# Kernel optimization log

Hardware: AMD Instinct MI355X
Metric: run time of the kernel (lower is better)

The kernel has to match this reference:

```python
import jax, jax.numpy as jnp
import numpy as np

H = W = 56
WS = 7          # window size
SHIFT = 3       # shift size
HEADS = 4
DIM = 128
NUM_MLP = 512
EPS = 1e-5


def _build_rel_index():
    ch = np.arange(WS)
    cw = np.arange(WS)
    coords = np.stack(np.meshgrid(ch, cw, indexing='ij')).reshape(2, -1)  # [2,49]
    rel = coords[:, :, None] - coords[:, None, :]                         # [2,49,49]
    rel = rel.transpose(1, 2, 0)
    rel[:, :, 0] += WS - 1
    rel[:, :, 1] += WS - 1
    rel[:, :, 0] *= 2 * WS - 1
    return rel.sum(-1).astype(np.int32)                                   # [49,49]


def _build_attn_mask():
    mask = np.zeros((H, W), dtype=np.float32)
    slices = (slice(0, -WS), slice(-WS, -SHIFT), slice(-SHIFT, None))
    cnt = 0
    for hs in slices:
        for ws_ in slices:
            mask[hs, ws_] = cnt
            cnt += 1
    nH, nW = H // WS, W // WS
    mw = mask.reshape(nH, WS, nW, WS).transpose(0, 2, 1, 3).reshape(nH * nW, WS * WS)
    am = mw[:, None, :] - mw[:, :, None]
    return np.where(am != 0, -100.0, 0.0).astype(np.float32)              # [64,49,49]


def setup_inputs() -> dict:
    key = jax.random.key(0)
    ks = jax.random.split(key, 8)
    B = 64
    s = 0.02
    return {
        'x': jax.random.normal(ks[0], (B, H * W, DIM), jnp.float32),
        'ln1_g': jnp.ones((DIM,), jnp.float32),
        'ln1_b': jnp.zeros((DIM,), jnp.float32),
        'eca_w': jax.random.normal(ks[1], (3, DIM, 1), jnp.float32) * s,
        'qkv_w': jax.random.normal(ks[2], (DIM, 3 * DIM), jnp.float32) * s,
        'qkv_b': jnp.zeros((3 * DIM,), jnp.float32),
        'rel_bias_table': jax.random.normal(ks[3], ((2 * WS - 1) ** 2, HEADS), jnp.float32) * s,
        'proj_w': jax.random.normal(ks[4], (DIM, DIM), jnp.float32) * s,
        'proj_b': jnp.zeros((DIM,), jnp.float32),
        'ln2_g': jnp.ones((DIM,), jnp.float32),
        'ln2_b': jnp.zeros((DIM,), jnp.float32),
        'mlp_w1': jax.random.normal(ks[5], (DIM, NUM_MLP), jnp.float32) * s,
        'mlp_b1': jnp.zeros((NUM_MLP,), jnp.float32),
        'mlp_w2': jax.random.normal(ks[6], (NUM_MLP, DIM), jnp.float32) * s,
        'mlp_b2': jnp.zeros((DIM,), jnp.float32),
        'attn_mask': jnp.asarray(_build_attn_mask()),
        'rel_index': jnp.asarray(_build_rel_index()),
    }


def _layer_norm(x, g, b):
    mu = x.mean(-1, keepdims=True)
    var = jnp.mean((x - mu) ** 2, -1, keepdims=True)
    return (x - mu) * jax.lax.rsqrt(var + EPS) * g + b


def _forward(x, ln1_g, ln1_b, eca_w, qkv_w, qkv_b, rel_bias_table, proj_w, proj_b,
             ln2_g, ln2_b, mlp_w1, mlp_b1, mlp_w2, mlp_b2, attn_mask, rel_index):
    B, L, C = x.shape
    nH, nW = H // WS, W // WS
    nwin = nH * nW
    hd = C // HEADS
    scale = hd ** -0.5

    x_skip = x
    xs = _layer_norm(x, ln1_g, ln1_b)
    x4 = xs.reshape(B, H, W, C)

    # Efficient channel attention (faithful: Conv1D over a length-1 steps axis,
    # 'same' padding -> only the center kernel tap contributes; gate is [B,1,1])
    sq = x4.mean((1, 2))[:, None, :]                                  # [B,1,C]
    gate = jax.lax.conv_general_dilated(
        sq, eca_w, (1,), 'SAME', dimension_numbers=('NWC', 'WIO', 'NWC'))  # [B,1,1]
    gate = jax.nn.sigmoid(gate)
    cattn = (x4 * gate[:, :, :, None]).reshape(B, H * W, C)

    # cyclic shift + window partition (batch-major, standard Swin layout)
    shifted = jnp.roll(x4, (-SHIFT, -SHIFT), (1, 2))
    xw = shifted.reshape(B, nH, WS, nW, WS, C).transpose(0, 1, 3, 2, 4, 5)
    xw = xw.reshape(B * nwin, WS * WS, C)                              # [Bn,49,C]

    # window attention with gathered relative position bias
    qkv = (xw @ qkv_w + qkv_b).reshape(-1, WS * WS, 3, HEADS, hd)
    qkv = qkv.transpose(2, 0, 3, 1, 4)                                 # [3,Bn,h,49,hd]
    q, k, v = qkv[0], qkv[1], qkv[2]
    attn = jnp.einsum('bhqd,bhkd->bhqk', q * scale, k)                 # [Bn,h,49,49]
    bias = rel_bias_table[rel_index.reshape(-1)]                       # [49*49,h]
    bias = bias.reshape(WS * WS, WS * WS, HEADS).transpose(2, 0, 1)    # [h,49,49]
    attn = attn + bias[None]
    attn = attn.reshape(B, nwin, HEADS, WS * WS, WS * WS) + attn_mask[None, :, None]
    attn = jax.nn.softmax(attn.reshape(-1, HEADS, WS * WS, WS * WS), -1)
    out = jnp.einsum('bhqk,bhkd->bqhd', attn, v).reshape(-1, WS * WS, C)
    out = out @ proj_w + proj_b                                        # [Bn,49,C]

    # window reverse + reverse shift
    out = out.reshape(B, nH, nW, WS, WS, C).transpose(0, 1, 3, 2, 4, 5)
    out = out.reshape(B, H, W, C)
    out = jnp.roll(out, (SHIFT, SHIFT), (1, 2)).reshape(B, H * W, C)

    x = x_skip + out + cattn
    x_skip = x
    xn = _layer_norm(x, ln2_g, ln2_b)
    h1 = jax.nn.gelu(xn @ mlp_w1 + mlp_b1, approximate=False)
    return x_skip + (h1 @ mlp_w2 + mlp_b2)


def reference(x, ln1_g, ln1_b, eca_w, qkv_w, qkv_b, rel_bias_table, proj_w, proj_b,
              ln2_g, ln2_b, mlp_w1, mlp_b1, mlp_w2, mlp_b2, attn_mask, rel_index):
    return _forward(x, ln1_g, ln1_b, eca_w, qkv_w, qkv_b, rel_bias_table, proj_w,
                    proj_b, ln2_g, ln2_b, mlp_w1, mlp_b1, mlp_w2, mlp_b2,
                    attn_mask, rel_index)
```

## Files before the change

kernel.cpp:

```cpp
#include <hip/hip_runtime.h>
#include <hip/hip_bf16.h>
#include <math.h>

#define B_    64
#define Himg  56
#define Wimg  56
#define L_    (Himg*Wimg)
#define WS_   7
#define SHIFT 3
#define NWIN  64
#define NTOK  49
#define HEADS 4
#define HD    32
#define DIM   128
#define NMLP  512
#define EPS   1e-5f
#define SCALE 0.17677669529663687f

typedef __hip_bfloat16 bf16;
typedef __attribute__((ext_vector_type(8))) short short8;
typedef __attribute__((ext_vector_type(4))) float floatx4;
typedef __attribute__((ext_vector_type(4))) unsigned short ushort4v;
#define MFMA16(a, b, c) __builtin_amdgcn_mfma_f32_16x16x32_bf16(a, b, c, 0, 0, 0)

__device__ float g_gacc[B_];
__device__ __align__(16) unsigned short g_w1t[NMLP * DIM];
__device__ __align__(16) unsigned short g_w2t[DIM * NMLP];
__device__ __align__(16) unsigned short g_qkvwt[3 * DIM * DIM];
__device__ __align__(16) unsigned short g_pwt[DIM * DIM];
__device__ float g_combo[NWIN * HEADS * NTOK * NTOK];

__device__ __forceinline__ float us2f(unsigned short u) {
  return __uint_as_float(((unsigned int)u) << 16);
}
__device__ __forceinline__ unsigned short f2us(float f) {
  unsigned int x = __float_as_uint(f);
  x += 0x7fffu + ((x >> 16) & 1u);
  return (unsigned short)(x >> 16);
}
__device__ __forceinline__ bool is_bf(const void* ones) {
  return ((const unsigned int*)ones)[0] == 0x3F803F80u;
}
template<bool BF>
__device__ __forceinline__ float ldf(const void* p, size_t i) {
  if (BF) return __bfloat162float(((const bf16*)p)[i]);
  return ((const float*)p)[i];
}
template<bool BF>
__device__ __forceinline__ floatx4 ld4(const void* p, size_t i) {
  if (BF) {
    const ushort4v u = *(const ushort4v*)((const unsigned short*)p + i);
    floatx4 r = {us2f(u.x), us2f(u.y), us2f(u.z), us2f(u.w)};
    return r;
  }
  return *(const floatx4*)((const float*)p + i);
}
template<bool BF>
__device__ __forceinline__ void st4(void* p, size_t i, floatx4 v) {
  if (BF) {
    ushort4v u = {f2us(v.x), f2us(v.y), f2us(v.z), f2us(v.w)};
    *(ushort4v*)((unsigned short*)p + i) = u;
  } else {
    *(floatx4*)((float*)p + i) = v;
  }
}
__device__ __forceinline__ float gelu_t(float x) {
  float y = 0.7978845608028654f * (x + 0.044715f * x * x * x);
  y = fminf(fmaxf(y, -15.f), 15.f);
  const float e = __expf(2.f * y);
  return 0.5f * x * (1.f + (e - 1.f) / (e + 1.f));
}

template<bool BF>
__global__ void k_prep(const void* __restrict__ w1, const void* __restrict__ w2,
                       const void* __restrict__ qkvw, const void* __restrict__ pw,
                       const void* __restrict__ rbt, const void* __restrict__ amask,
                       const int* __restrict__ ridx, const void* __restrict__ ones) {
  if (is_bf(ones) != BF) return;
  const int bid = blockIdx.x, tid = threadIdx.x;
  if (bid == 0 && tid < B_) g_gacc[tid] = 0.f;
  if (bid < 256) {
    const int idx = bid * 256 + tid;
    { const int k = idx >> 9, n = idx & 511; g_w1t[n * DIM + k] = f2us(ldf<BF>(w1, idx)); }
    { const int k = idx >> 7, n = idx & 127; g_w2t[n * NMLP + k] = f2us(ldf<BF>(w2, idx)); }
  } else if (bid < 448) {
    const int idx = (bid - 256) * 256 + tid;
    { const int k = idx / 384, n = idx % 384; g_qkvwt[n * DIM + k] = f2us(ldf<BF>(qkvw, idx)); }
    if (idx < DIM * DIM) {
      const int k = idx >> 7, n = idx & 127;
      g_pwt[n * DIM + k] = f2us(ldf<BF>(pw, idx));
    }
  } else {
    const int wh_ = bid - 448;
    const int widx = wh_ >> 2, h = wh_ & 3;
    for (int idx = tid; idx < NTOK * NTOK; idx += 256) {
      g_combo[(size_t)wh_ * (NTOK * NTOK) + idx] =
          ldf<BF>(rbt, (size_t)ridx[idx] * HEADS + h) +
          ldf<BF>(amask, (size_t)widx * (NTOK * NTOK) + idx);
    }
  }
}

template<bool BF>
__global__ void k_gate_partial(const void* __restrict__ x,
                               const void* __restrict__ ln1_g,
                               const void* __restrict__ ln1_b,
                               const void* __restrict__ eca_w) {
  if (is_bf(ln1_g) != BF) return;
  const int b = blockIdx.x;
  const int lane = threadIdx.x & 63;
  const int wave = threadIdx.x >> 6;
  const int c4 = (lane & 31) * 4;
  const floatx4 g4  = ld4<BF>(ln1_g, c4);
  const floatx4 be4 = ld4<BF>(ln1_b, c4);
  const floatx4 w4  = ld4<BF>(eca_w, DIM + c4);
  float acc = 0.f;
  const int t0 = blockIdx.y * 8 + wave * 2 + (lane >> 5);
  for (int t = t0; t < L_; t += 64) {
    const floatx4 v = ld4<BF>(x, ((size_t)b * L_ + t) * DIM + c4);
    float s = v.x + v.y + v.z + v.w;
    float s2 = v.x * v.x + v.y * v.y + v.z * v.z + v.w * v.w;
    #pragma unroll
    for (int m = 1; m <= 16; m <<= 1) {
      s  += __shfl_xor(s,  m, 64);
      s2 += __shfl_xor(s2, m, 64);
    }
    const float mu = s * (1.f / DIM);
    const float rs = rsqrtf(s2 * (1.f / DIM) - mu * mu + EPS);
    acc += ((v.x - mu) * rs * g4.x + be4.x) * w4.x
         + ((v.y - mu) * rs * g4.y + be4.y) * w4.y
         + ((v.z - mu) * rs * g4.z + be4.z) * w4.z
         + ((v.w - mu) * rs * g4.w + be4.w) * w4.w;
  }
  #pragma unroll
  for (int m = 1; m <= 32; m <<= 1) acc += __shfl_xor(acc, m, 64);
  if (lane == 0) atomicAdd(&g_gacc[b], acc);
}

template<bool BF>
__global__ __launch_bounds__(512, 4) void k_attn_mfma(
    const void* __restrict__ x,
    const void* __restrict__ ln1_g, const void* __restrict__ ln1_b,
    const void* __restrict__ qkv_b, const void* __restrict__ proj_b,
    void* __restrict__ x2) {
  if (is_bf(ln1_g) != BF) return;
  __shared__ __align__(16) unsigned short q_s[NTOK * 136];
  __shared__ __align__(16) unsigned short k_s[NTOK * 136];
  __shared__ __align__(16) unsigned short xno[NTOK * 136];
  __shared__ __align__(16) unsigned short vt[128 * 72];
  __shared__ __align__(16) unsigned short Pb[8 * 16 * 40];
  __shared__ float mu[NTOK], rs[NTOK];
  unsigned short* o_s = q_s;

  const int tid = threadIdx.x;
  const int bw = blockIdx.x;
  const int b = bw >> 6, widx = bw & 63;
  const int wh = widx >> 3, wc = widx & 7;
  const int w = tid >> 6, l = tid & 63;
  const int pair = w >> 1, p = w & 1;
  const int lr = l & 15, lq = l >> 4;

  for (int idx = tid; idx < 128 * 16; idx += 512)
    vt[(idx >> 4) * 72 + 48 + (idx & 15)] = 0;
  for (int idx = tid; idx < NTOK * 32; idx += 512) {
    const int i = idx >> 5, c4 = (idx & 31) * 4;
    const int r = i / 7, qq = i % 7;
    const int oh = (wh * 7 + r + SHIFT) % Himg;
    const int ow = (wc * 7 + qq + SHIFT) % Wimg;
    const floatx4 v = ld4<BF>(x, ((size_t)b * L_ + oh * Wimg + ow) * DIM + c4);
    ushort4v u = {f2us(v.x), f2us(v.y), f2us(v.z), f2us(v.w)};
    *(ushort4v*)&xno[i * 136 + c4] = u;
  }
  __syncthreads();
  {
    const int i = tid >> 3, c0 = (tid & 7) * 16;
    if (i < NTOK) {
      const short8 r0 = *(const short8*)&xno[i * 136 + c0];
      const short8 r1 = *(const short8*)&xno[i * 136 + c0 + 8];
      float s = 0.f, s2 = 0.f;
      #pragma unroll
      for (int j = 0; j < 8; j++) {
        const float a = us2f((unsigned short)r0[j]);
        const float c = us2f((unsigned short)r1[j]);
        s += a + c; s2 += a * a + c * c;
      }
      s  += __shfl_xor(s, 1, 64);  s  += __shfl_xor(s, 2, 64);  s  += __shfl_xor(s, 4, 64);
      s2 += __shfl_xor(s2, 1, 64); s2 += __shfl_xor(s2, 2, 64); s2 += __shfl_xor(s2, 4, 64);
      if ((tid & 7) == 0) {
        const float m = s * (1.f / DIM);
        mu[i] = m;
        rs[i] = rsqrtf(s2 * (1.f / DIM) - m * m + EPS);
      }
    }
  }
  __syncthreads();
  for (int idx = tid; idx < NTOK * 16; idx += 512) {
    const int i = idx >> 4, c8 = (idx & 15) * 8;
    const floatx4 g0 = ld4<BF>(ln1_g, c8), g1 = ld4<BF>(ln1_g, c8 + 4);
    const floatx4 b0 = ld4<BF>(ln1_b, c8), b1 = ld4<BF>(ln1_b, c8 + 4);
    const short8 a = *(const short8*)&xno[i * 136 + c8];
    const float m = mu[i], rr = rs[i];
    short8 o;
    o[0] = (short)f2us((us2f((unsigned short)a[0]) - m) * rr * g0.x + b0.x);
    o[1] = (short)f2us((us2f((unsigned short)a[1]) - m) * rr * g0.y + b0.y);
    o[2] = (short)f2us((us2f((unsigned short)a[2]) - m) * rr * g0.z + b0.z);
    o[3] = (short)f2us((us2f((unsigned short)a[3]) - m) * rr * g0.w + b0.w);
    o[4] = (short)f2us((us2f((unsigned short)a[4]) - m) * rr * g1.x + b1.x);
    o[5] = (short)f2us((us2f((unsigned short)a[5]) - m) * rr * g1.y + b1.y);
    o[6] = (short)f2us((us2f((unsigned short)a[6]) - m) * rr * g1.z + b1.z);
    o[7] = (short)f2us((us2f((unsigned short)a[7]) - m) * rr * g1.w + b1.w);
    *(short8*)&xno[i * 136 + c8] = o;
  }
  __syncthreads();

  {
    const int mp = p;
    for (int np = 0; np < 3; np++) {
      const int n0 = pair * 96 + np * 32 + lr;
      const int n1 = n0 + 16;
      floatx4 a00 = {0.f, 0.f, 0.f, 0.f}, a01 = a00, a10 = a00, a11 = a00;
      #pragma unroll
      for (int kc = 0; kc < 4; kc++) {
        const int k0 = kc * 32 + lq * 8;
        const short8 A0 = *(const short8*)&xno[(mp * 32 + lr) * 136 + k0];
        const short8 A1 = *(const short8*)&xno[(mp * 32 + 16 + lr) * 136 + k0];
        const short8 B0 = *(const short8*)&g_qkvwt[n0 * DIM + k0];
        const short8 B1 = *(const short8*)&g_qkvwt[n1 * DIM + k0];
        a00 = MFMA16(A0, B0, a00); a01 = MFMA16(A0, B1, a01);
        a10 = MFMA16(A1, B0, a10); a11 = MFMA16(A1, B1, a11);
      }
      const float bb0 = ldf<BF>(qkv_b, n0), bb1 = ldf<BF>(qkv_b, n1);
      #pragma unroll
      for (int r = 0; r < 4; r++) {
        const int i0 = mp * 32 + lq * 4 + r, i1 = i0 + 16;
        #pragma unroll
        for (int t = 0; t < 4; t++) {
          const int i = (t & 2) ? i1 : i0;
          const int n = (t & 1) ? n1 : n0;
          const float val = (t == 0 ? a00[r] : t == 1 ? a01[r] : t == 2 ? a10[r] : a11[r])
                            + ((t & 1) ? bb1 : bb0);
          if (i < NTOK) {
            const unsigned short hv = f2us(val);
            if (n < DIM) q_s[i * 136 + n] = hv;
            else if (n < 2 * DIM) k_s[i * 136 + (n - DIM)] = hv;
            else vt[(n - 2 * DIM) * 72 + i] = hv;
          }
        }
      }
    }
  }
  __syncthreads();

  {
    const int h = pair;
    unsigned short* Pw = &Pb[w * 16 * 40];
    const size_t cbase = (size_t)((widx << 2) + h) * (NTOK * NTOK);
    for (int mm = 0; mm < 2; mm++) {
      const int mi = p * 2 + mm;
      const short8 Aq = *(const short8*)&q_s[(mi * 16 + lr) * 136 + h * 32 + lq * 8];
      float sv[4][4];
      #pragma unroll
      for (int ni = 0; ni < 4; ni++) {
        const short8 Bk = *(const short8*)&k_s[(ni * 16 + lr) * 136 + h * 32 + lq * 8];
        floatx4 z = {0.f, 0.f, 0.f, 0.f};
        const floatx4 sc = MFMA16(Aq, Bk, z);
        const int j = ni * 16 + lr;
        #pragma unroll
        for (int r = 0; r < 4; r++) {
          const int i = mi * 16 + lq * 4 + r;
          float s = -1e30f;
          if (i < NTOK && j < NTOK)
            s = sc[r] * SCALE + g_combo[cbase + i * NTOK + j];
          sv[ni][r] = s;
        }
      }
      float inv[4];
      #pragma unroll
      for (int r = 0; r < 4; r++) {
        float m = fmaxf(fmaxf(sv[0][r], sv[1][r]), fmaxf(sv[2][r], sv[3][r]));
        m = fmaxf(m, __shfl_xor(m, 1, 64)); m = fmaxf(m, __shfl_xor(m, 2, 64));
        m = fmaxf(m, __shfl_xor(m, 4, 64)); m = fmaxf(m, __shfl_xor(m, 8, 64));
        float s = 0.f;
        #pragma unroll
        for (int ni = 0; ni < 4; ni++) { sv[ni][r] = __expf(sv[ni][r] - m); s += sv[ni][r]; }
        s += __shfl_xor(s, 1, 64); s += __shfl_xor(s, 2, 64);
        s += __shfl_xor(s, 4, 64); s += __shfl_xor(s, 8, 64);
        inv[r] = 1.f / s;
      }
      floatx4 o0 = {0.f, 0.f, 0.f, 0.f}, o1 = o0;
      #pragma unroll
      for (int kq = 0; kq < 2; kq++) {
        #pragma unroll
        for (int nn = 0; nn < 2; nn++) {
          const int ni = kq * 2 + nn;
          #pragma unroll
          for (int r = 0; r < 4; r++)
            Pw[(lq * 4 + r) * 40 + nn * 16 + lr] = f2us(sv[ni][r] * inv[r]);
        }
        const short8 Ap  = *(const short8*)&Pw[lr * 40 + lq * 8];
        const short8 Bv0 = *(const short8*)&vt[(h * 32 + lr) * 72 + kq * 32 + lq * 8];
        const short8 Bv1 = *(const short8*)&vt[(h * 32 + 16 + lr) * 72 + kq * 32 + lq * 8];
        o0 = MFMA16(Ap, Bv0, o0);
        o1 = MFMA16(Ap, Bv1, o1);
      }
      #pragma unroll
      for (int r = 0; r < 4; r++) {
        const int i = mi * 16 + lq * 4 + r;
        if (i < NTOK) {
          xno[i * 136 + h * 32 + lr]      = f2us(o0[r]);
          xno[i * 136 + h * 32 + 16 + lr] = f2us(o1[r]);
        }
      }
    }
  }
  __syncthreads();

  {
    const int mp = p;
    const int n0 = pair * 32 + lr, n1 = n0 + 16;
    floatx4 a00 = {0.f, 0.f, 0.f, 0.f}, a01 = a00, a10 = a00, a11 = a00;
    #pragma unroll
    for (int kc = 0; kc < 4; kc++) {
      const int k0 = kc * 32 + lq * 8;
      const short8 A0 = *(const short8*)&xno[(mp * 32 + lr) * 136 + k0];
      const short8 A1 = *(const short8*)&xno[(mp * 32 + 16 + lr) * 136 + k0];
      const short8 B0 = *(const short8*)&g_pwt[n0 * DIM + k0];
      const short8 B1 = *(const short8*)&g_pwt[n1 * DIM + k0];
      a00 = MFMA16(A0, B0, a00); a01 = MFMA16(A0, B1, a01);
      a10 = MFMA16(A1, B0, a10); a11 = MFMA16(A1, B1, a11);
    }
    const float pb0 = ldf<BF>(proj_b, n0), pb1 = ldf<BF>(proj_b, n1);
    #pragma unroll
    for (int r = 0; r < 4; r++) {
      const int i0 = mp * 32 + lq * 4 + r, i1 = i0 + 16;
      if (i0 < NTOK) {
        o_s[i0 * 136 + n0] = f2us(a00[r] + pb0);
        o_s[i0 * 136 + n1] = f2us(a01[r] + pb1);
      }
      if (i1 < NTOK) {
        o_s[i1 * 136 + n0] = f2us(a10[r] + pb0);
        o_s[i1 * 136 + n1] = f2us(a11[r] + pb1);
      }
    }
  }
  __syncthreads();
  {
    const float gb = 1.f / (1.f + __expf(-g_gacc[b] * (1.f / (float)L_)));
    for (int idx = tid; idx < NTOK * 32; idx += 512) {
      const int i = idx >> 5, c4 = (idx & 31) * 4;
      const int r = i / 7, qq = i % 7;
      const int oh = (wh * 7 + r + SHIFT) % Himg;
      const int ow = (wc * 7 + qq + SHIFT) % Wimg;
      const size_t pos = ((size_t)b * L_ + oh * Wimg + ow) * DIM + c4;
      const floatx4 xv = ld4<BF>(x, pos);
      const ushort4v o4 = *(const ushort4v*)&o_s[i * 136 + c4];
      const floatx4 g4 = ld4<BF>(ln1_g, c4);
      const floatx4 b4 = ld4<BF>(ln1_b, c4);
      const float m = mu[i], rr = rs[i];
      floatx4 out;
      out.x = xv.x + us2f(o4.x) + gb * ((xv.x - m) * rr * g4.x + b4.x);
      out.y = xv.y + us2f(o4.y) + gb * ((xv.y - m) * rr * g4.y + b4.y);
      out.z = xv.z + us2f(o4.z) + gb * ((xv.z - m) * rr * g4.z + b4.z);
      out.w = xv.w + us2f(o4.w) + gb * ((xv.w - m) * rr * g4.w + b4.w);
      st4<BF>(x2, pos, out);
    }
  }
}

template<bool BF>
__global__ __launch_bounds__(512, 4) void k_mlp_mfma(
    const void* __restrict__ ln2_g, const void* __restrict__ ln2_b,
    const void* __restrict__ b1v, const void* __restrict__ b2v,
    void* __restrict__ io) {
  if (is_bf(ln2_g) != BF) return;
  __shared__ __align__(16) unsigned short xn[32][136];
  __shared__ __align__(16) unsigned short h1[32][520];
  const int tid = threadIdx.x;
  const size_t t0 = (size_t)blockIdx.x * 32;
  const int w = tid >> 6, l = tid & 63;
  const int lr = l & 15, lq = l >> 4;

  {
    const int i = tid >> 4, c0 = (tid & 15) * 8;
    const size_t base = (t0 + i) * DIM + c0;
    const floatx4 va = ld4<BF>(io, base);
    const floatx4 vb = ld4<BF>(io, base + 4);
    float s = va.x + va.y + va.z + va.w + vb.x + vb.y + vb.z + vb.w;
    float s2 = va.x * va.x + va.y * va.y + va.z * va.z + va.w * va.w
             + vb.x * vb.x + vb.y * vb.y + vb.z * vb.z + vb.w * vb.w;
    s  += __shfl_xor(s, 1, 64);  s  += __shfl_xor(s, 2, 64);
    s  += __shfl_xor(s, 4, 64);  s  += __shfl_xor(s, 8, 64);
    s2 += __shfl_xor(s2, 1, 64); s2 += __shfl_xor(s2, 2, 64);
    s2 += __shfl_xor(s2, 4, 64); s2 += __shfl_xor(s2, 8, 64);
    const float m = s * (1.f / DIM);
    const float rr = rsqrtf(s2 * (1.f / DIM) - m * m + EPS);
    const floatx4 g0 = ld4<BF>(ln2_g, c0), g1 = ld4<BF>(ln2_g, c0 + 4);
    const floatx4 e0 = ld4<BF>(ln2_b, c0), e1 = ld4<BF>(ln2_b, c0 + 4);
    short8 o;
    o[0] = (short)f2us((va.x - m) * rr * g0.x + e0.x);
    o[1] = (short)f2us((va.y - m) * rr * g0.y + e0.y);
    o[2] = (short)f2us((va.z - m) * rr * g0.z + e0.z);
    o[3] = (short)f2us((va.w - m) * rr * g0.w + e0.w);
    o[4] = (short)f2us((vb.x - m) * rr * g1.x + e1.x);
    o[5] = (short)f2us((vb.y - m) * rr * g1.y + e1.y);
    o[6] = (short)f2us((vb.z - m) * rr * g1.z + e1.z);
    o[7] = (short)f2us((vb.w - m) * rr * g1.w + e1.w);
    *(short8*)&xn[i][c0] = o;
  }
  __syncthreads();

  #pragma unroll
  for (int np = 0; np < 2; np++) {
    const int nc0 = w * 64 + np * 32 + lr;
    const int nc1 = nc0 + 16;
    floatx4 a00 = {0.f, 0.f, 0.f, 0.f}, a01 = a00, a10 = a00, a11 = a00;
    #pragma unroll
    for (int kc = 0; kc < 4; kc++) {
      const int k0 = kc * 32 + lq * 8;
      const short8 A0 = *(const short8*)&xn[lr][k0];
      const short8 A1 = *(const short8*)&xn[lr + 16][k0];
      const short8 B0 = *(const short8*)&g_w1t[nc0 * DIM + k0];
      const short8 B1 = *(const short8*)&g_w1t[nc1 * DIM + k0];
      a00 = MFMA16(A0, B0, a00); a01 = MFMA16(A0, B1, a01);
      a10 = MFMA16(A1, B0, a10); a11 = MFMA16(A1, B1, a11);
    }
    const float bb0 = ldf<BF>(b1v, nc0);
    const float bb1 = ldf<BF>(b1v, nc1);
    #pragma unroll
    for (int r = 0; r < 4; r++) {
      const int row = lq * 4 + r;
      h1[row][nc0]      = f2us(gelu_t(a00[r] + bb0));
      h1[row][nc1]      = f2us(gelu_t(a01[r] + bb1));
      h1[row + 16][nc0] = f2us(gelu_t(a10[r] + bb0));
      h1[row + 16][nc1] = f2us(gelu_t(a11[r] + bb1));
    }
  }
  __syncthreads();

  {
    const int nc = w * 16 + lr;
    floatx4 a0 = {0.f, 0.f, 0.f, 0.f}, a1 = a0;
    #pragma unroll
    for (int kc = 0; kc < 16; kc++) {
      const int k0 = kc * 32 + lq * 8;
      const short8 A0 = *(const short8*)&h1[lr][k0];
      const short8 A1 = *(const short8*)&h1[lr + 16][k0];
      const short8 B0 = *(const short8*)&g_w2t[nc * NMLP + k0];
      a0 = MFMA16(A0, B0, a0);
      a1 = MFMA16(A1, B0, a1);
    }
    const float bb = ldf<BF>(b2v, nc);
    #pragma unroll
    for (int r = 0; r < 4; r++) {
      const int row = lq * 4 + r;
      xn[row][nc]      = f2us(a0[r] + bb);
      xn[row + 16][nc] = f2us(a1[r] + bb);
    }
  }
  __syncthreads();

  for (int idx = tid; idx < 32 * 32; idx += 512) {
    const int i = idx >> 5, c4 = (idx & 31) * 4;
    const size_t pos = (t0 + i) * DIM + c4;
    const floatx4 v = ld4<BF>(io, pos);
    const ushort4v o4 = *(const ushort4v*)&xn[i][c4];
    floatx4 out = {v.x + us2f(o4.x), v.y + us2f(o4.y),
                   v.z + us2f(o4.z), v.w + us2f(o4.w)};
    st4<BF>(io, pos, out);
  }
}

extern "C" void kernel_launch(void* const* d_in, const int* in_sizes, int n_in,
                              void* d_out, int out_size, void* d_ws, size_t ws_size,
                              hipStream_t stream) {
  const void* x     = d_in[0];
  const void* ln1g  = d_in[1];
  const void* ln1b  = d_in[2];
  const void* ecaw  = d_in[3];
  const void* qkvw  = d_in[4];
  const void* qkvb  = d_in[5];
  const void* rbt   = d_in[6];
  const void* projw = d_in[7];
  const void* projb = d_in[8];
  const void* ln2g  = d_in[9];
  const void* ln2b  = d_in[10];
  const void* w1    = d_in[11];
  const void* b1    = d_in[12];
  const void* w2    = d_in[13];
  const void* b2    = d_in[14];
  const void* amask = d_in[15];
  const int*  ridx  = (const int*)d_in[16];

  const int gsz = in_sizes[1];
  const bool launch_bf = (gsz != 512);
  const bool launch_fp = (gsz != 256);

  if (launch_bf) k_prep<true ><<<704, 256, 0, stream>>>(w1, w2, qkvw, projw, rbt, amask, ridx, ln1g);
  if (launch_fp) k_prep<false><<<704, 256, 0, stream>>>(w1, w2, qkvw, projw, rbt, amask, ridx, ln1g);
  if (launch_bf) k_gate_partial<true ><<<dim3(B_, 8), 256, 0, stream>>>(x, ln1g, ln1b, ecaw);
  if (launch_fp) k_gate_partial<false><<<dim3(B_, 8), 256, 0, stream>>>(x, ln1g, ln1b, ecaw);
  if (launch_bf) k_attn_mfma<true ><<<B_ * NWIN, 512, 0, stream>>>(x, ln1g, ln1b, qkvb, projb, d_out);
  if (launch_fp) k_attn_mfma<false><<<B_ * NWIN, 512, 0, stream>>>(x, ln1g, ln1b, qkvb, projb, d_out);
  if (launch_bf) k_mlp_mfma<true ><<<(B_ * L_) / 32, 512, 0, stream>>>(ln2g, ln2b, b1, b2, d_out);
  if (launch_fp) k_mlp_mfma<false><<<(B_ * L_) / 32, 512, 0, stream>>>(ln2g, ln2b, b1, b2, d_out);
}
```

Before: 655.1 us.

## Double MLP token tile to 64 and stream hidden dim in halves

```diff
diff --git a/kernel.cpp b/kernel.cpp
--- a/kernel.cpp
+++ b/kernel.cpp
@@ -368,98 +368,132 @@
 }
 
 template<bool BF>
-__global__ __launch_bounds__(512, 4) void k_mlp_mfma(
+__global__ __launch_bounds__(512, 6) void k_mlp_mfma(
     const void* __restrict__ ln2_g, const void* __restrict__ ln2_b,
     const void* __restrict__ b1v, const void* __restrict__ b2v,
     void* __restrict__ io) {
   if (is_bf(ln2_g) != BF) return;
-  __shared__ __align__(16) unsigned short xn[32][136];
-  __shared__ __align__(16) unsigned short h1[32][520];
+  __shared__ __align__(16) unsigned short xn[64][136];
+  __shared__ __align__(16) unsigned short h1[64][264];
   const int tid = threadIdx.x;
-  const size_t t0 = (size_t)blockIdx.x * 32;
+  const size_t t0 = (size_t)blockIdx.x * 64;
   const int w = tid >> 6, l = tid & 63;
   const int lr = l & 15, lq = l >> 4;
 
   {
-    const int i = tid >> 4, c0 = (tid & 15) * 8;
+    const int i = tid >> 3, c0 = (tid & 7) * 16;
     const size_t base = (t0 + i) * DIM + c0;
     const floatx4 va = ld4<BF>(io, base);
     const floatx4 vb = ld4<BF>(io, base + 4);
-    float s = va.x + va.y + va.z + va.w + vb.x + vb.y + vb.z + vb.w;
+    const floatx4 vc = ld4<BF>(io, base + 8);
+    const floatx4 vd = ld4<BF>(io, base + 12);
+    float s = va.x + va.y + va.z + va.w + vb.x + vb.y + vb.z + vb.w
+            + vc.x + vc.y + vc.z + vc.w + vd.x + vd.y + vd.z + vd.w;
     float s2 = va.x * va.x + va.y * va.y + va.z * va.z + va.w * va.w
-             + vb.x * vb.x + vb.y * vb.y + vb.z * vb.z + vb.w * vb.w;
-    s  += __shfl_xor(s, 1, 64);  s  += __shfl_xor(s, 2, 64);
-    s  += __shfl_xor(s, 4, 64);  s  += __shfl_xor(s, 8, 64);
-    s2 += __shfl_xor(s2, 1, 64); s2 += __shfl_xor(s2, 2, 64);
-    s2 += __shfl_xor(s2, 4, 64); s2 += __shfl_xor(s2, 8, 64);
+             + vb.x * vb.x + vb.y * vb.y + vb.z * vb.z + vb.w * vb.w
+             + vc.x * vc.x + vc.y * vc.y + vc.z * vc.z + vc.w * vc.w
+             + vd.x * vd.x + vd.y * vd.y + vd.z * vd.z + vd.w * vd.w;
+    s  += __shfl_xor(s, 1, 64);  s  += __shfl_xor(s, 2, 64);  s  += __shfl_xor(s, 4, 64);
+    s2 += __shfl_xor(s2, 1, 64); s2 += __shfl_xor(s2, 2, 64); s2 += __shfl_xor(s2, 4, 64);
     const float m = s * (1.f / DIM);
     const float rr = rsqrtf(s2 * (1.f / DIM) - m * m + EPS);
-    const floatx4 g0 = ld4<BF>(ln2_g, c0), g1 = ld4<BF>(ln2_g, c0 + 4);
-    const floatx4 e0 = ld4<BF>(ln2_b, c0), e1 = ld4<BF>(ln2_b, c0 + 4);
-    short8 o;
-    o[0] = (short)f2us((va.x - m) * rr * g0.x + e0.x);
-    o[1] = (short)f2us((va.y - m) * rr * g0.y + e0.y);
-    o[2] = (short)f2us((va.z - m) * rr * g0.z + e0.z);
-    o[3] = (short)f2us((va.w - m) * rr * g0.w + e0.w);
-    o[4] = (short)f2us((vb.x - m) * rr * g1.x + e1.x);
-    o[5] = (short)f2us((vb.y - m) * rr * g1.y + e1.y);
-    o[6] = (short)f2us((vb.z - m) * rr * g1.z + e1.z);
-    o[7] = (short)f2us((vb.w - m) * rr * g1.w + e1.w);
-    *(short8*)&xn[i][c0] = o;
-  }
-  __syncthreads();
+    const floatx4 g0 = ld4<BF>(ln2_g, c0),     g1 = ld4<BF>(ln2_g, c0 + 4);
+    const floatx4 g2 = ld4<BF>(ln2_g, c0 + 8), g3 = ld4<BF>(ln2_g, c0 + 12);
+    const floatx4 e0 = ld4<BF>(ln2_b, c0),     e1 = ld4<BF>(ln2_b, c0 + 4);
+    const floatx4 e2 = ld4<BF>(ln2_b, c0 + 8), e3 = ld4<BF>(ln2_b, c0 + 12);
+    short8 o0, o1;
+    o0[0] = (short)f2us((va.x - m) * rr * g0.x + e0.x);
+    o0[1] = (short)f2us((va.y - m) * rr * g0.y + e0.y);
+    o0[2] = (short)f2us((va.z - m) * rr * g0.z + e0.z);
+    o0[3] = (short)f2us((va.w - m) * rr * g0.w + e0.w);
+    o0[4] = (short)f2us((vb.x - m) * rr * g1.x + e1.x);
+    o0[5] = (short)f2us((vb.y - m) * rr * g1.y + e1.y);
+    o0[6] = (short)f2us((vb.z - m) * rr * g1.z + e1.z);
+    o0[7] = (short)f2us((vb.w - m) * rr * g1.w + e1.w);
+    o1[0] = (short)f2us((vc.x - m) * rr * g2.x + e2.x);
+    o1[1] = (short)f2us((vc.y - m) * rr * g2.y + e2.y);
+    o1[2] = (short)f2us((vc.z - m) * rr * g2.z + e2.z);
+    o1[3] = (short)f2us((vc.w - m) * rr * g2.w + e2.w);
+    o1[4] = (short)f2us((vd.x - m) * rr * g3.x + e3.x);
+    o1[5] = (short)f2us((vd.y - m) * rr * g3.y + e3.y);
+    o1[6] = (short)f2us((vd.z - m) * rr * g3.z + e3.z);
+    o1[7] = (short)f2us((vd.w - m) * rr * g3.w + e3.w);
+    *(short8*)&xn[i][c0] = o0;
+    *(short8*)&xn[i][c0 + 8] = o1;
+  }
+  __syncthreads();
+
+  floatx4 c2[4] = {{0.f, 0.f, 0.f, 0.f}, {0.f, 0.f, 0.f, 0.f},
+                   {0.f, 0.f, 0.f, 0.f}, {0.f, 0.f, 0.f, 0.f}};
 
   #pragma unroll
-  for (int np = 0; np < 2; np++) {
-    const int nc0 = w * 64 + np * 32 + lr;
-    const int nc1 = nc0 + 16;
-    floatx4 a00 = {0.f, 0.f, 0.f, 0.f}, a01 = a00, a10 = a00, a11 = a00;
-    #pragma unroll
-    for (int kc = 0; kc < 4; kc++) {
-      const int k0 = kc * 32 + lq * 8;
-      const short8 A0 = *(const short8*)&xn[lr][k0];
-      const short8 A1 = *(const short8*)&xn[lr + 16][k0];
-      const short8 B0 = *(const short8*)&g_w1t[nc0 * DIM + k0];
-      const short8 B1 = *(const short8*)&g_w1t[nc1 * DIM + k0];
-      a00 = MFMA16(A0, B0, a00); a01 = MFMA16(A0, B1, a01);
-      a10 = MFMA16(A1, B0, a10); a11 = MFMA16(A1, B1, a11);
-    }
-    const float bb0 = ldf<BF>(b1v, nc0);
-    const float bb1 = ldf<BF>(b1v, nc1);
-    #pragma unroll
-    for (int r = 0; r < 4; r++) {
-      const int row = lq * 4 + r;
-      h1[row][nc0]      = f2us(gelu_t(a00[r] + bb0));
-      h1[row][nc1]      = f2us(gelu_t(a01[r] + bb1));
-      h1[row + 16][nc0] = f2us(gelu_t(a10[r] + bb0));
-      h1[row + 16][nc1] = f2us(gelu_t(a11[r] + bb1));
-    }
-  }
-  __syncthreads();
+  for (int half = 0; half < 2; half++) {
+    {
+      const int n0 = half * 256 + w * 32 + lr;
+      const int n1 = n0 + 16;
+      floatx4 a0[4] = {{0.f, 0.f, 0.f, 0.f}, {0.f, 0.f, 0.f, 0.f},
+                       {0.f, 0.f, 0.f, 0.f}, {0.f, 0.f, 0.f, 0.f}};
+      floatx4 a1[4] = {{0.f, 0.f, 0.f, 0.f}, {0.f, 0.f, 0.f, 0.f},
+                       {0.f, 0.f, 0.f, 0.f}, {0.f, 0.f, 0.f, 0.f}};
+      #pragma unroll
+      for (int kc = 0; kc < 4; kc++) {
+        const int k0 = kc * 32 + lq * 8;
+        const short8 B0 = *(const short8*)&g_w1t[n0 * DIM + k0];
+        const short8 B1 = *(const short8*)&g_w1t[n1 * DIM + k0];
+        #pragma unroll
+        for (int mt = 0; mt < 4; mt++) {
+          const short8 A = *(const short8*)&xn[mt * 16 + lr][k0];
+          a0[mt] = MFMA16(A, B0, a0[mt]);
+          a1[mt] = MFMA16(A, B1, a1[mt]);
+        }
+      }
+      const float bb0 = ldf<BF>(b1v, n0);
+      const float bb1 = ldf<BF>(b1v, n1);
+      const int hc0 = w * 32 + lr;
+      #pragma unroll
+      for (int mt = 0; mt < 4; mt++) {
+        #pragma unroll
+        for (int r = 0; r < 4; r++) {
+          const int row = mt * 16 + lq * 4 + r;
+          h1[row][hc0]      = f2us(gelu_t(a0[mt][r] + bb0));
+          h1[row][hc0 + 16] = f2us(gelu_t(a1[mt][r] + bb1));
+        }
+      }
+    }
+    __syncthreads();
+
+    {
+      const int nc = w * 16 + lr;
+      const int kb = half * 256;
+      #pragma unroll
+      for (int kc = 0; kc < 8; kc++) {
+        const int k0 = kc * 32 + lq * 8;
+        const short8 B = *(const short8*)&g_w2t[nc * NMLP + kb + k0];
+        #pragma unroll
+        for (int mt = 0; mt < 4; mt++) {
+          const short8 A = *(const short8*)&h1[mt * 16 + lr][k0];
+          c2[mt] = MFMA16(A, B, c2[mt]);
+        }
+      }
+    }
+    __syncthreads();
+  }
 
   {
     const int nc = w * 16 + lr;
-    floatx4 a0 = {0.f, 0.f, 0.f, 0.f}, a1 = a0;
-    #pragma unroll
-    for (int kc = 0; kc < 16; kc++) {
-      const int k0 = kc * 32 + lq * 8;
-      const short8 A0 = *(const short8*)&h1[lr][k0];
-      const short8 A1 = *(const short8*)&h1[lr + 16][k0];
-      const short8 B0 = *(const short8*)&g_w2t[nc * NMLP + k0];
-      a0 = MFMA16(A0, B0, a0);
-      a1 = MFMA16(A1, B0, a1);
-    }
     const float bb = ldf<BF>(b2v, nc);
     #pragma unroll
-    for (int r = 0; r < 4; r++) {
-      const int row = lq * 4 + r;
-      xn[row][nc]      = f2us(a0[r] + bb);
-      xn[row + 16][nc] = f2us(a1[r] + bb);
-    }
-  }
-  __syncthreads();
-
-  for (int idx = tid; idx < 32 * 32; idx += 512) {
+    for (int mt = 0; mt < 4; mt++) {
+      #pragma unroll
+      for (int r = 0; r < 4; r++) {
+        const int row = mt * 16 + lq * 4 + r;
+        xn[row][nc] = f2us(c2[mt][r] + bb);
+      }
+    }
+  }
+  __syncthreads();
+
+  for (int idx = tid; idx < 64 * 32; idx += 512) {
     const int i = idx >> 5, c4 = (idx & 31) * 4;
     const size_t pos = (t0 + i) * DIM + c4;
     const floatx4 v = ld4<BF>(io, pos);
@@ -501,6 +535,6 @@
   if (launch_fp) k_gate_partial<false><<<dim3(B_, 8), 256, 0, stream>>>(x, ln1g, ln1b, ecaw);
   if (launch_bf) k_attn_mfma<true ><<<B_ * NWIN, 512, 0, stream>>>(x, ln1g, ln1b, qkvb, projb, d_out);
   if (launch_fp) k_attn_mfma<false><<<B_ * NWIN, 512, 0, stream>>>(x, ln1g, ln1b, qkvb, projb, d_out);
-  if (launch_bf) k_mlp_mfma<true ><<<(B_ * L_) / 32, 512, 0, stream>>>(ln2g, ln2b, b1, b2, d_out);
-  if (launch_fp) k_mlp_mfma<false><<<(B_ * L_) / 32, 512, 0, stream>>>(ln2g, ln2b, b1, b2, d_out);
-}
+  if (launch_bf) k_mlp_mfma<true ><<<(B_ * L_) / 64, 512, 0, stream>>>(ln2g, ln2b, b1, b2, d_out);
+  if (launch_fp) k_mlp_mfma<false><<<(B_ * L_) / 64, 512, 0, stream>>>(ln2g, ln2b, b1, b2, d_out);
+}
```

Result: faster. 590.4 us (-9.9%).
